# Optimization experiments

Hardware: AMD Instinct MI355X
Metric: run time of the kernel (lower is better)

## Reference

```python
import jax, jax.numpy as jnp
import numpy as np

N_PTS = 1_000_000
B = 2048          # number of graphs
C_IN = 8
C_OUT = 32        # `channel` trivial irreps -> conv/activation width
WIDTH = 4.0       # kernel radial width
N_RINGS = 2
EPS = 1e-6


def setup_inputs() -> dict:
    key = jax.random.key(0)
    k = jax.random.split(key, 6)
    x = jax.random.normal(k[0], (N_PTS, C_IN), dtype=jnp.float32)
    coords = jax.random.normal(k[1], (N_PTS, 3), dtype=jnp.float32)
    batch = jnp.sort(jax.random.randint(k[2], (N_PTS,), 0, B))
    # steerable kernel weights: [C_out, C_in, n_rings * n_angular(=4: Y0 + Y1)]
    W = jax.random.normal(k[3], (C_OUT, C_IN, N_RINGS * 4), dtype=jnp.float32) * 0.1
    gamma = jnp.ones((C_OUT,), dtype=jnp.float32)
    beta = jnp.zeros((C_OUT,), dtype=jnp.float32)
    act_bias = jax.random.uniform(k[4], (C_OUT,), dtype=jnp.float32)
    return {"x": x, "coords": coords, "batch": batch, "W": W,
            "gamma": gamma, "beta": beta, "act_bias": act_bias}


def reference(x, coords, batch, W, gamma, beta, act_bias):
    n = x.shape[0]
    # --- global_mean_pool of coords per graph -> out_coords [B,3] ---
    cnt = jax.ops.segment_sum(jnp.ones((n,), x.dtype), batch, num_segments=B)
    cnt = jnp.maximum(cnt, 1.0)
    pos = jax.ops.segment_sum(coords, batch, num_segments=B) / cnt[:, None]
    # --- per-edge relative position: edge i = (point i -> center of graph batch[i]) ---
    rel = pos[batch] - coords                    # [N,3] gather (irregular access)
    d = jnp.linalg.norm(rel, axis=-1)            # [N]
    # --- radial Gaussian ring profile ---
    rings = jnp.linspace(0.0, WIDTH, N_RINGS)
    sigma = WIDTH / max(N_RINGS - 1, 1)
    radial = jnp.exp(-0.5 * ((d[:, None] - rings[None, :]) / sigma) ** 2)   # [N,R]
    # --- angular part: real spherical harmonics l=0 (const) and l=1 (direction) ---
    direc = rel / jnp.maximum(d, EPS)[:, None]
    ang = jnp.concatenate([jnp.ones((n, 1), x.dtype), direc], axis=-1)      # [N,4]
    basis = (radial[:, :, None] * ang[:, None, :]).reshape(n, -1)           # [N, R*4]
    # --- continuous-kernel point conv: per-edge kernel eval + message ---
    msg = jnp.einsum('eb,oib,ei->eo', basis, W, x)                          # [N,C_out]
    # --- scatter-add aggregation to graph centers ---
    out = jax.ops.segment_sum(msg, batch, num_segments=B)                   # [B,C_out]
    # --- IID batch norm (per-channel, batch statistics) ---
    mu = out.mean(axis=0)
    var = out.var(axis=0)
    out = (out - mu) / jnp.sqrt(var + 1e-5) * gamma + beta
    # --- NormNonLinearity (trivial fields) followed by NormPool: relu(|x| - b) ---
    y = jax.nn.relu(jnp.abs(out) - act_bias)                                # [B,C_out]
    return y
```

## Files before the change

kernel.cpp:

```cpp
#include <hip/hip_runtime.h>


#define RS8_STAGE(M, HALF)                                  \
  {                                                         \
    const bool hi_ = (lane & (M)) != 0;                     \
    _Pragma("unroll")                                       \
    for (int k = 0; k < (HALF); ++k) {                      \
      float send = hi_ ? acc[k] : acc[(HALF) + k];          \
      float keep = hi_ ? acc[(HALF) + k] : acc[k];          \
      acc[k] = keep + __shfl_xor(send, (M), 64);            \
    }                                                       \
  }

#define NBLK_STATS 64

__device__ __forceinline__ int rev3(int s) {
  return ((s & 1) << 2) | (s & 2) | ((s & 4) >> 2);
}

__device__ __forceinline__ void basis8(float rx, float ry, float rz,
                                       float* bas) {
  float d2 = rx * rx + ry * ry + rz * rz;
  float d = sqrtf(d2);
  float r0 = __expf(-0.03125f * d2);
  float tt = (d - 4.0f) * 0.25f;
  float r1 = __expf(-0.5f * tt * tt);
  float idm = 1.0f / fmaxf(d, 1e-6f);
  float ax = rx * idm, ay = ry * idm, az = rz * idm;
  bas[0] = r0; bas[1] = r0 * ax; bas[2] = r0 * ay; bas[3] = r0 * az;
  bas[4] = r1; bas[5] = r1 * ax; bas[6] = r1 * ay; bas[7] = r1 * az;
}

__device__ __forceinline__ int lower_bound64(const int* __restrict__ a,
                                             int n, int key, int lane) {
  int lo = 0, len = n;
  while (len > 64) {
    int chunk = (len + 63) >> 6;
    int p = lo + lane * chunk;
    bool c = (p < lo + len) && (a[p] < key);
    unsigned long long mask = __ballot(c);
    int m = __popcll(mask);
    if (m == 0) { len = 0; break; }
    int nlo = lo + (m - 1) * chunk + 1;
    int nhi = min(lo + m * chunk, lo + len);
    lo = nlo;
    len = nhi - nlo;
  }
  if (len > 0) {
    int p = lo + lane;
    bool c = (lane < len) && (a[p] < key);
    lo += __popcll(__ballot(c));
  }
  return lo;
}

__global__ __launch_bounds__(256) void graph_kernel(
    const float* __restrict__ x, const float* __restrict__ coords,
    const int* __restrict__ batch, const float* __restrict__ W,
    float* __restrict__ out_raw, int n) {
  __shared__ __align__(16) float pv[4][64][20];
  __shared__ float sredm[4][3];
  __shared__ float sred[4][64];
  __shared__ float sVg[64];
  __shared__ float pre2[4][32];
  __shared__ float smean[3];
  __shared__ int sbound[2];

  const int g = blockIdx.x;
  const int t = threadIdx.x;
  const int lane = t & 63;
  const int wv = t >> 6;

  if (wv < 2) {
    int r = lower_bound64(batch, n, g + wv, lane);
    if (lane == 0) sbound[wv] = r;
  }
  __syncthreads();
  const int lo = sbound[0], hi = sbound[1];
  const int cnt = hi - lo;

  float s1 = 0.f, s2 = 0.f, s3 = 0.f;
  for (int i = lo + t; i < hi; i += 256) {
    s1 += coords[(size_t)i * 3 + 0];
    s2 += coords[(size_t)i * 3 + 1];
    s3 += coords[(size_t)i * 3 + 2];
  }
#pragma unroll
  for (int m = 1; m < 64; m <<= 1) {
    s1 += __shfl_xor(s1, m, 64);
    s2 += __shfl_xor(s2, m, 64);
    s3 += __shfl_xor(s3, m, 64);
  }
  if (lane == 0) { sredm[wv][0] = s1; sredm[wv][1] = s2; sredm[wv][2] = s3; }
  __syncthreads();
  if (t < 3) {
    smean[t] = (sredm[0][t] + sredm[1][t] + sredm[2][t] + sredm[3][t]) /
               (float)max(cnt, 1);
  }
  __syncthreads();
  const float mx = smean[0], my = smean[1], mz = smean[2];

  const int i8 = lane >> 3;
  const int sub = lane & 7;
  float acc[8];
#pragma unroll
  for (int b = 0; b < 8; ++b) acc[b] = 0.f;

  const int niter = (cnt + 255) >> 8;
  for (int it = 0; it < niter; ++it) {
    const int ip = lo + it * 256 + wv * 64 + lane;
    const bool vp = ip < hi;
    const int ic = min(ip, n - 1);
    float cx = coords[(size_t)ic * 3 + 0];
    float cy = coords[(size_t)ic * 3 + 1];
    float cz = coords[(size_t)ic * 3 + 2];
    float bas[8];
    basis8(mx - cx, my - cy, mz - cz, bas);
    float4 xa = ((const float4*)x)[2 * (size_t)ic];
    float4 xb = ((const float4*)x)[2 * (size_t)ic + 1];
    if (!vp) {
      xa = make_float4(0.f, 0.f, 0.f, 0.f);
      xb = make_float4(0.f, 0.f, 0.f, 0.f);
    }
    float* dst = &pv[wv][lane][0];
    ((float4*)dst)[0] = xa;
    ((float4*)dst)[1] = xb;
    ((float4*)dst)[2] = make_float4(bas[0], bas[1], bas[2], bas[3]);
    ((float4*)dst)[3] = make_float4(bas[4], bas[5], bas[6], bas[7]);
#pragma unroll
    for (int j = 0; j < 8; ++j) {
      const float* src = &pv[wv][8 * j + sub][0];
      float xvv = src[i8];
      float4 b03 = *(const float4*)(src + 8);
      float4 b47 = *(const float4*)(src + 12);
      acc[0] += xvv * b03.x;
      acc[1] += xvv * b03.y;
      acc[2] += xvv * b03.z;
      acc[3] += xvv * b03.w;
      acc[4] += xvv * b47.x;
      acc[5] += xvv * b47.y;
      acc[6] += xvv * b47.z;
      acc[7] += xvv * b47.w;
    }
  }

  RS8_STAGE(1, 4)
  RS8_STAGE(2, 2)
  RS8_STAGE(4, 1)
  sred[wv][i8 * 8 + rev3(sub)] = acc[0];
  __syncthreads();
  if (t < 64) sVg[t] = sred[0][t] + sred[1][t] + sred[2][t] + sred[3][t];
  __syncthreads();

  const int o = t & 31;
  const int part = t >> 5;
  const float* wrow = W + (size_t)o * 64 + part * 8;
  float4 w0 = *(const float4*)(wrow);
  float4 w1 = *(const float4*)(wrow + 4);
  float4 v0 = *(const float4*)(&sVg[part * 8]);
  float4 v1 = *(const float4*)(&sVg[part * 8 + 4]);
  float r = w0.x * v0.x + w0.y * v0.y + w0.z * v0.z + w0.w * v0.w +
            w1.x * v1.x + w1.y * v1.y + w1.z * v1.z + w1.w * v1.w;
  r += __shfl_xor(r, 32, 64);
  if (lane < 32) pre2[wv][o] = r;
  __syncthreads();
  if (t < 32) {
    out_raw[(size_t)g * 32 + t] =
        pre2[0][t] + pre2[1][t] + pre2[2][t] + pre2[3][t];
  }
}

__global__ __launch_bounds__(256) void stats_kernel(
    const float* __restrict__ out_raw, float* __restrict__ spart, int B) {
  __shared__ float red[4][32], redq[4][32];
  const int t = threadIdx.x;
  const int o = t & 31;
  const int lane = t & 63;
  const int wv = t >> 6;
  const int stride = NBLK_STATS * 256;
  float s = 0.f, q = 0.f;
  for (int e = blockIdx.x * 256 + t; e < B * 32; e += stride) {
    float val = out_raw[e];
    s += val;
    q += val * val;
  }
  s += __shfl_xor(s, 32, 64);
  q += __shfl_xor(q, 32, 64);
  if (lane < 32) { red[wv][o] = s; redq[wv][o] = q; }
  __syncthreads();
  if (t < 32) {
    spart[blockIdx.x * 64 + t] =
        red[0][t] + red[1][t] + red[2][t] + red[3][t];
    spart[blockIdx.x * 64 + 32 + t] =
        redq[0][t] + redq[1][t] + redq[2][t] + redq[3][t];
  }
}

__global__ __launch_bounds__(256) void final_kernel(
    const float* __restrict__ out_raw, const float* __restrict__ spart,
    const float* __restrict__ gamma, const float* __restrict__ beta,
    const float* __restrict__ act_bias, float* __restrict__ out, int B) {
  __shared__ float ssums[64];
  __shared__ float sscale[32], sshift[32], sbias[32];
  const int t = threadIdx.x;
  const int total = B * 32;

  if (t < 64) {
    float s = 0.f;
#pragma unroll 8
    for (int b = 0; b < NBLK_STATS; ++b) s += spart[b * 64 + t];
    ssums[t] = s;
  }
  __syncthreads();
  if (t < 32) {
    float invB = 1.0f / (float)B;
    float mu = ssums[t] * invB;
    float var = ssums[32 + t] * invB - mu * mu;
    float sc = rsqrtf(var + 1e-5f) * gamma[t];
    sscale[t] = sc;
    sshift[t] = beta[t] - mu * sc;
    sbias[t]  = act_bias[t];
  }
  __syncthreads();

  const int base = (blockIdx.x * 256 + t) * 4;
  if (base < total) {
    float4 vv = *(const float4*)(out_raw + base);
    const int o0 = base & 31;
    float r0 = fabsf(vv.x * sscale[o0 + 0] + sshift[o0 + 0]) - sbias[o0 + 0];
    float r1 = fabsf(vv.y * sscale[o0 + 1] + sshift[o0 + 1]) - sbias[o0 + 1];
    float r2 = fabsf(vv.z * sscale[o0 + 2] + sshift[o0 + 2]) - sbias[o0 + 2];
    float r3 = fabsf(vv.w * sscale[o0 + 3] + sshift[o0 + 3]) - sbias[o0 + 3];
    *(float4*)(out + base) = make_float4(fmaxf(r0, 0.f), fmaxf(r1, 0.f),
                                         fmaxf(r2, 0.f), fmaxf(r3, 0.f));
  }
}

extern "C" void kernel_launch(void* const* d_in, const int* in_sizes, int n_in,
                              void* d_out, int out_size, void* d_ws, size_t ws_size,
                              hipStream_t stream) {
  const float* x      = (const float*)d_in[0];
  const float* coords = (const float*)d_in[1];
  const int*   batch  = (const int*)d_in[2];
  const float* W      = (const float*)d_in[3];
  const float* gamma  = (const float*)d_in[4];
  const float* beta   = (const float*)d_in[5];
  const float* abias  = (const float*)d_in[6];
  float* out = (float*)d_out;

  int n = in_sizes[2];
  int B = out_size / 32;

  float* out_raw = (float*)d_ws;
  float* spart   = out_raw + (size_t)B * 32;

  graph_kernel<<<B, 256, 0, stream>>>(x, coords, batch, W, out_raw, n);
  stats_kernel<<<NBLK_STATS, 256, 0, stream>>>(out_raw, spart, B);
  int nblk_final = (B * 32 + 1023) / 1024;
  final_kernel<<<nblk_final, 256, 0, stream>>>(out_raw, spart, gamma, beta, abias, out, B);
}
```

Before: 30.02 us.

## Assign one wavefront per graph instead of one block per graph

Restructures graph_kernel so each 64-lane wavefront handles a whole graph, packing four graphs per 256-thread block and launching a quarter as many blocks. This removes every __syncthreads and the cross-wave shared-memory reductions for the centroid, the basis accumulation and the W projection. Each wave now runs both binary searches itself and walks its graph's ~488 points 64 at a time, so per-graph latency is longer and there is less parallelism inside each graph.

```diff
diff --git a/kernel.cpp b/kernel.cpp
--- a/kernel.cpp
+++ b/kernel.cpp
@@ -57,30 +57,22 @@
 __global__ __launch_bounds__(256) void graph_kernel(
     const float* __restrict__ x, const float* __restrict__ coords,
     const int* __restrict__ batch, const float* __restrict__ W,
-    float* __restrict__ out_raw, int n) {
+    float* __restrict__ out_raw, int n, int B) {
   __shared__ __align__(16) float pv[4][64][20];
-  __shared__ float sredm[4][3];
-  __shared__ float sred[4][64];
-  __shared__ float sVg[64];
-  __shared__ float pre2[4][32];
-  __shared__ float smean[3];
-  __shared__ int sbound[2];
-
-  const int g = blockIdx.x;
+  __shared__ float sVg[4][64];
+
   const int t = threadIdx.x;
   const int lane = t & 63;
   const int wv = t >> 6;
-
-  if (wv < 2) {
-    int r = lower_bound64(batch, n, g + wv, lane);
-    if (lane == 0) sbound[wv] = r;
-  }
-  __syncthreads();
-  const int lo = sbound[0], hi = sbound[1];
+  const int g = blockIdx.x * 4 + wv;
+  if (g >= B) return;
+
+  const int lo = lower_bound64(batch, n, g, lane);
+  const int hi = lower_bound64(batch, n, g + 1, lane);
   const int cnt = hi - lo;
 
   float s1 = 0.f, s2 = 0.f, s3 = 0.f;
-  for (int i = lo + t; i < hi; i += 256) {
+  for (int i = lo + lane; i < hi; i += 64) {
     s1 += coords[(size_t)i * 3 + 0];
     s2 += coords[(size_t)i * 3 + 1];
     s3 += coords[(size_t)i * 3 + 2];
@@ -91,14 +83,8 @@
     s2 += __shfl_xor(s2, m, 64);
     s3 += __shfl_xor(s3, m, 64);
   }
-  if (lane == 0) { sredm[wv][0] = s1; sredm[wv][1] = s2; sredm[wv][2] = s3; }
-  __syncthreads();
-  if (t < 3) {
-    smean[t] = (sredm[0][t] + sredm[1][t] + sredm[2][t] + sredm[3][t]) /
-               (float)max(cnt, 1);
-  }
-  __syncthreads();
-  const float mx = smean[0], my = smean[1], mz = smean[2];
+  const float inv = 1.0f / (float)max(cnt, 1);
+  const float mx = s1 * inv, my = s2 * inv, mz = s3 * inv;
 
   const int i8 = lane >> 3;
   const int sub = lane & 7;
@@ -106,9 +92,9 @@
 #pragma unroll
   for (int b = 0; b < 8; ++b) acc[b] = 0.f;
 
-  const int niter = (cnt + 255) >> 8;
+  const int niter = (cnt + 63) >> 6;
   for (int it = 0; it < niter; ++it) {
-    const int ip = lo + it * 256 + wv * 64 + lane;
+    const int ip = lo + it * 64 + lane;
     const bool vp = ip < hi;
     const int ic = min(ip, n - 1);
     float cx = coords[(size_t)ic * 3 + 0];
@@ -147,27 +133,21 @@
   RS8_STAGE(1, 4)
   RS8_STAGE(2, 2)
   RS8_STAGE(4, 1)
-  sred[wv][i8 * 8 + rev3(sub)] = acc[0];
-  __syncthreads();
-  if (t < 64) sVg[t] = sred[0][t] + sred[1][t] + sred[2][t] + sred[3][t];
-  __syncthreads();
-
-  const int o = t & 31;
-  const int part = t >> 5;
-  const float* wrow = W + (size_t)o * 64 + part * 8;
-  float4 w0 = *(const float4*)(wrow);
-  float4 w1 = *(const float4*)(wrow + 4);
-  float4 v0 = *(const float4*)(&sVg[part * 8]);
-  float4 v1 = *(const float4*)(&sVg[part * 8 + 4]);
-  float r = w0.x * v0.x + w0.y * v0.y + w0.z * v0.z + w0.w * v0.w +
-            w1.x * v1.x + w1.y * v1.y + w1.z * v1.z + w1.w * v1.w;
+  sVg[wv][i8 * 8 + rev3(sub)] = acc[0];
+
+  const int o = lane & 31;
+  const int part = lane >> 5;
+  const float* wrow = W + (size_t)o * 64 + part * 32;
+  const float* vrow = &sVg[wv][part * 32];
+  float r = 0.f;
+#pragma unroll
+  for (int c = 0; c < 8; ++c) {
+    float4 w4 = *(const float4*)(wrow + c * 4);
+    float4 v4 = *(const float4*)(vrow + c * 4);
+    r += w4.x * v4.x + w4.y * v4.y + w4.z * v4.z + w4.w * v4.w;
+  }
   r += __shfl_xor(r, 32, 64);
-  if (lane < 32) pre2[wv][o] = r;
-  __syncthreads();
-  if (t < 32) {
-    out_raw[(size_t)g * 32 + t] =
-        pre2[0][t] + pre2[1][t] + pre2[2][t] + pre2[3][t];
-  }
+  if (lane < 32) out_raw[(size_t)g * 32 + o] = r;
 }
 
 __global__ __launch_bounds__(256) void stats_kernel(
@@ -254,7 +234,8 @@
   float* out_raw = (float*)d_ws;
   float* spart   = out_raw + (size_t)B * 32;
 
-  graph_kernel<<<B, 256, 0, stream>>>(x, coords, batch, W, out_raw, n);
+  int nblk_graph = (B + 3) / 4;
+  graph_kernel<<<nblk_graph, 256, 0, stream>>>(x, coords, batch, W, out_raw, n, B);
   stats_kernel<<<NBLK_STATS, 256, 0, stream>>>(out_raw, spart, B);
   int nblk_final = (B * 32 + 1023) / 1024;
   final_kernel<<<nblk_final, 256, 0, stream>>>(out_raw, spart, gamma, beta, abias, out, B);
```

After: 30.32 us. About the same (+1.0%).

## Fuse stats and final kernels via grid barrier; widen per-lane accumulator tile

Applied to the files above, without the earlier changes.

Merges the batch-norm statistics kernel and the normalize/activation kernel into a single 64-block launch. The blocks synchronize through a global atomic counter spin barrier, and the counter is reset by the first graph block. Separately, the per-wave inner product now has each lane accumulate two input channels (16 accumulators, float2 loads, 4 iterations instead of 8), which cuts LDS reads and adds one reduction stage. The spin barrier assumes all 64 blocks are co-resident, and the larger accumulator count raises register pressure.

```diff
diff --git a/kernel.cpp b/kernel.cpp
--- a/kernel.cpp
+++ b/kernel.cpp
@@ -1,7 +1,7 @@
 #include <hip/hip_runtime.h>
 
 
-#define RS8_STAGE(M, HALF)                                  \
+#define RS16_STAGE(M, HALF)                                 \
   {                                                         \
     const bool hi_ = (lane & (M)) != 0;                     \
     _Pragma("unroll")                                       \
@@ -12,10 +12,8 @@
     }                                                       \
   }
 
-#define NBLK_STATS 64
-
-__device__ __forceinline__ int rev3(int s) {
-  return ((s & 1) << 2) | (s & 2) | ((s & 4) >> 2);
+__device__ __forceinline__ int rev4(int s) {
+  return ((s & 1) << 3) | ((s & 2) << 1) | ((s & 4) >> 1) | ((s & 8) >> 3);
 }
 
 __device__ __forceinline__ void basis8(float rx, float ry, float rz,
@@ -57,7 +55,7 @@
 __global__ __launch_bounds__(256) void graph_kernel(
     const float* __restrict__ x, const float* __restrict__ coords,
     const int* __restrict__ batch, const float* __restrict__ W,
-    float* __restrict__ out_raw, int n) {
+    float* __restrict__ out_raw, int* __restrict__ counter, int n) {
   __shared__ __align__(16) float pv[4][64][20];
   __shared__ float sredm[4][3];
   __shared__ float sred[4][64];
@@ -71,6 +69,8 @@
   const int lane = t & 63;
   const int wv = t >> 6;
 
+  if (g == 0 && t == 0) *(volatile int*)counter = 0;
+
   if (wv < 2) {
     int r = lower_bound64(batch, n, g + wv, lane);
     if (lane == 0) sbound[wv] = r;
@@ -100,11 +100,11 @@
   __syncthreads();
   const float mx = smean[0], my = smean[1], mz = smean[2];
 
-  const int i8 = lane >> 3;
-  const int sub = lane & 7;
-  float acc[8];
+  const int q2 = lane >> 4;
+  const int sub = lane & 15;
+  float acc[16];
 #pragma unroll
-  for (int b = 0; b < 8; ++b) acc[b] = 0.f;
+  for (int b = 0; b < 16; ++b) acc[b] = 0.f;
 
   const int niter = (cnt + 255) >> 8;
   for (int it = 0; it < niter; ++it) {
@@ -128,26 +128,27 @@
     ((float4*)dst)[2] = make_float4(bas[0], bas[1], bas[2], bas[3]);
     ((float4*)dst)[3] = make_float4(bas[4], bas[5], bas[6], bas[7]);
 #pragma unroll
-    for (int j = 0; j < 8; ++j) {
-      const float* src = &pv[wv][8 * j + sub][0];
-      float xvv = src[i8];
+    for (int j = 0; j < 4; ++j) {
+      const float* src = &pv[wv][16 * j + sub][0];
+      float2 xp = *(const float2*)(src + 2 * q2);
       float4 b03 = *(const float4*)(src + 8);
       float4 b47 = *(const float4*)(src + 12);
-      acc[0] += xvv * b03.x;
-      acc[1] += xvv * b03.y;
-      acc[2] += xvv * b03.z;
-      acc[3] += xvv * b03.w;
-      acc[4] += xvv * b47.x;
-      acc[5] += xvv * b47.y;
-      acc[6] += xvv * b47.z;
-      acc[7] += xvv * b47.w;
+      acc[0]  += xp.x * b03.x;  acc[1]  += xp.x * b03.y;
+      acc[2]  += xp.x * b03.z;  acc[3]  += xp.x * b03.w;
+      acc[4]  += xp.x * b47.x;  acc[5]  += xp.x * b47.y;
+      acc[6]  += xp.x * b47.z;  acc[7]  += xp.x * b47.w;
+      acc[8]  += xp.y * b03.x;  acc[9]  += xp.y * b03.y;
+      acc[10] += xp.y * b03.z;  acc[11] += xp.y * b03.w;
+      acc[12] += xp.y * b47.x;  acc[13] += xp.y * b47.y;
+      acc[14] += xp.y * b47.z;  acc[15] += xp.y * b47.w;
     }
   }
 
-  RS8_STAGE(1, 4)
-  RS8_STAGE(2, 2)
-  RS8_STAGE(4, 1)
-  sred[wv][i8 * 8 + rev3(sub)] = acc[0];
+  RS16_STAGE(1, 8)
+  RS16_STAGE(2, 4)
+  RS16_STAGE(4, 2)
+  RS16_STAGE(8, 1)
+  sred[wv][16 * q2 + rev4(sub)] = acc[0];
   __syncthreads();
   if (t < 64) sVg[t] = sred[0][t] + sred[1][t] + sred[2][t] + sred[3][t];
   __syncthreads();
@@ -170,16 +171,22 @@
   }
 }
 
-__global__ __launch_bounds__(256) void stats_kernel(
-    const float* __restrict__ out_raw, float* __restrict__ spart, int B) {
+__global__ __launch_bounds__(256) void statsfinal_kernel(
+    const float* __restrict__ out_raw, float* __restrict__ spart,
+    int* __restrict__ counter, const float* __restrict__ gamma,
+    const float* __restrict__ beta, const float* __restrict__ act_bias,
+    float* __restrict__ out, int B) {
   __shared__ float red[4][32], redq[4][32];
+  __shared__ float ssums[64];
+  __shared__ float sscale[32], sshift[32], sbias[32];
   const int t = threadIdx.x;
   const int o = t & 31;
   const int lane = t & 63;
   const int wv = t >> 6;
-  const int stride = NBLK_STATS * 256;
+  const int total = B * 32;
+
   float s = 0.f, q = 0.f;
-  for (int e = blockIdx.x * 256 + t; e < B * 32; e += stride) {
+  for (int e = blockIdx.x * 256 + t; e < total; e += 64 * 256) {
     float val = out_raw[e];
     s += val;
     q += val * val;
@@ -193,23 +200,21 @@
         red[0][t] + red[1][t] + red[2][t] + red[3][t];
     spart[blockIdx.x * 64 + 32 + t] =
         redq[0][t] + redq[1][t] + redq[2][t] + redq[3][t];
-  }
-}
-
-__global__ __launch_bounds__(256) void final_kernel(
-    const float* __restrict__ out_raw, const float* __restrict__ spart,
-    const float* __restrict__ gamma, const float* __restrict__ beta,
-    const float* __restrict__ act_bias, float* __restrict__ out, int B) {
-  __shared__ float ssums[64];
-  __shared__ float sscale[32], sshift[32], sbias[32];
-  const int t = threadIdx.x;
-  const int total = B * 32;
+    __threadfence();
+  }
+  __syncthreads();
+  if (t == 0) {
+    atomicAdd(counter, 1);
+    while (atomicAdd(counter, 0) < 64) __builtin_amdgcn_s_sleep(2);
+  }
+  __syncthreads();
+  __threadfence();
 
   if (t < 64) {
-    float s = 0.f;
+    float sum = 0.f;
 #pragma unroll 8
-    for (int b = 0; b < NBLK_STATS; ++b) s += spart[b * 64 + t];
-    ssums[t] = s;
+    for (int b = 0; b < 64; ++b) sum += ((volatile float*)spart)[b * 64 + t];
+    ssums[t] = sum;
   }
   __syncthreads();
   if (t < 32) {
@@ -223,8 +228,8 @@
   }
   __syncthreads();
 
-  const int base = (blockIdx.x * 256 + t) * 4;
-  if (base < total) {
+  for (int base = (blockIdx.x * 256 + t) * 4; base < total;
+       base += 64 * 256 * 4) {
     float4 vv = *(const float4*)(out_raw + base);
     const int o0 = base & 31;
     float r0 = fabsf(vv.x * sscale[o0 + 0] + sshift[o0 + 0]) - sbias[o0 + 0];
@@ -253,9 +258,9 @@
 
   float* out_raw = (float*)d_ws;
   float* spart   = out_raw + (size_t)B * 32;
-
-  graph_kernel<<<B, 256, 0, stream>>>(x, coords, batch, W, out_raw, n);
-  stats_kernel<<<NBLK_STATS, 256, 0, stream>>>(out_raw, spart, B);
-  int nblk_final = (B * 32 + 1023) / 1024;
-  final_kernel<<<nblk_final, 256, 0, stream>>>(out_raw, spart, gamma, beta, abias, out, B);
-}
+  int*   counter = (int*)(spart + 64 * 64);
+
+  graph_kernel<<<B, 256, 0, stream>>>(x, coords, batch, W, out_raw, counter, n);
+  statsfinal_kernel<<<64, 256, 0, stream>>>(out_raw, spart, counter, gamma,
+                                            beta, abias, out, B);
+}
```

After: 46.49 us. +54.8%, slower.
